# Optimization experiments

Hardware: AMD Instinct MI355X
Metric: run time of the kernel (lower is better)

The kernel has to match this reference:

```python
import jax, jax.numpy as jnp
import numpy as np

EMBED = 1024
HEADS = 16
HEAD_DIM = EMBED // HEADS
SCALING = HEAD_DIM ** -0.5
R = 16
LORA_SCALE = 32.0 / R  # alpha / r
NEG = jnp.finfo(jnp.float32).min


def lora_linear(x, W, A, B):
    # y = x @ W.T + (x @ A.T) @ B.T * scale   (LinearLora, bias=False)
    return x @ W.T + ((x @ A.T) @ B.T) * LORA_SCALE


def setup_inputs() -> dict:
    key = jax.random.key(0)
    ks = jax.random.split(key, 14)
    B, T, D = 1, 4096, EMBED
    hidden_states = jax.random.normal(ks[0], (B, T, D), jnp.float32)
    # causal additive mask (bsz, 1, tgt, src): 0 on/below diag, dtype-min above
    i = jnp.arange(T)
    causal = jnp.where(i[:, None] >= i[None, :], 0.0, NEG).astype(jnp.float32)
    attention_mask = jnp.broadcast_to(causal, (B, 1, T, T))
    s = 0.02
    def w(k, shape):
        return jax.random.normal(k, shape, jnp.float32) * s
    return dict(
        hidden_states=hidden_states,
        attention_mask=attention_mask,
        Wq=w(ks[1], (D, D)), Wk=w(ks[2], (D, D)), Wv=w(ks[3], (D, D)), Wo=w(ks[4], (D, D)),
        Aq=w(ks[5], (R, D)), Bq=jnp.zeros((D, R), jnp.float32) + w(ks[6], (D, R)),
        Ak=w(ks[7], (R, D)), Bk=w(ks[8], (D, R)),
        Av=w(ks[9], (R, D)), Bv=w(ks[10], (D, R)),
        Ao=w(ks[11], (R, D)), Bo=w(ks[12], (D, R)),
    )


def reference(hidden_states, attention_mask, Wq, Wk, Wv, Wo,
              Aq, Bq, Ak, Bk, Av, Bv, Ao, Bo):
    bsz, tgt_len, _ = hidden_states.shape
    H, Hd = HEADS, HEAD_DIM

    q = lora_linear(hidden_states, Wq, Aq, Bq) * SCALING
    k = lora_linear(hidden_states, Wk, Ak, Bk)
    v = lora_linear(hidden_states, Wv, Av, Bv)

    # (b, t, H, Hd)
    q = q.reshape(bsz, tgt_len, H, Hd)
    k = k.reshape(bsz, tgt_len, H, Hd)
    v = v.reshape(bsz, tgt_len, H, Hd)

    # scores (b, H, t, s)
    attn = jnp.einsum('bthd,bshd->bhts', q, k)
    attn = attn + attention_mask
    attn = jnp.maximum(attn, NEG)
    attn = jax.nn.softmax(attn, axis=-1)  # dropout p=0 / eval mode

    out = jnp.einsum('bhts,bshd->bthd', attn, v)
    out = out.reshape(bsz, tgt_len, H * Hd)
    out = lora_linear(out, Wo, Ao, Bo)
    return out
```

## Files before the change

kernel.cpp:

```cpp
#include <hip/hip_runtime.h>
#include <cmath>
#include <cstdint>

typedef unsigned short u16;
typedef __attribute__((ext_vector_type(8))) __bf16 bf16x8;
typedef __attribute__((ext_vector_type(4))) __bf16 bf16x4;
typedef __attribute__((ext_vector_type(4))) short s16x4;
typedef __attribute__((ext_vector_type(4))) float f32x4;

__device__ __forceinline__ u16 f2bf(float f) {
    union { float f; unsigned u; } v; v.f = f;
    unsigned r = v.u + 0x7fffu + ((v.u >> 16) & 1u);
    return (u16)(r >> 16);
}

__device__ __forceinline__ void gload_lds(const u16* g, u16* l) {
    __builtin_amdgcn_global_load_lds((__attribute__((address_space(1))) void*)g,
                                     (__attribute__((address_space(3))) void*)l,
                                     16, 0, 0);
}

__device__ __forceinline__ f32x4 mfma16(s16x4 a, s16x4 b, f32x4 c) {
#if __has_builtin(__builtin_amdgcn_mfma_f32_16x16x16bf16_1k)
    return __builtin_amdgcn_mfma_f32_16x16x16bf16_1k(a, b, c, 0, 0, 0);
#else
    asm("v_mfma_f32_16x16x16_bf16 %0, %1, %2, %3"
        : "=v"(c) : "v"(a), "v"(b), "0"(c));
    return c;
#endif
}

__global__ __launch_bounds__(256) void prep_all(
        const float* __restrict__ X,
        const float* __restrict__ Wq, const float* __restrict__ Wk,
        const float* __restrict__ Wv, const float* __restrict__ Wo,
        const float* __restrict__ Aq, const float* __restrict__ Bq,
        const float* __restrict__ Ak, const float* __restrict__ Bk,
        const float* __restrict__ Av, const float* __restrict__ Bv,
        const float* __restrict__ Ao, const float* __restrict__ Bo,
        u16* __restrict__ Wqkv, u16* __restrict__ Wob, u16* __restrict__ Xb) {
    const int p = blockIdx.y;
    const int idx = blockIdx.x * 256 + threadIdx.x;
    if (p == 4) {
        float4 v = ((const float4*)X)[idx];
        ushort4 o;
        o.x = f2bf(v.x); o.y = f2bf(v.y); o.z = f2bf(v.z); o.w = f2bf(v.w);
        ((ushort4*)Xb)[idx] = o;
        return;
    }
    const int n = idx >> 10, d = idx & 1023;
    const float* W; const float* A; const float* B;
    switch (p) {
        case 0: W = Wq; A = Aq; B = Bq; break;
        case 1: W = Wk; A = Ak; B = Bk; break;
        case 2: W = Wv; A = Av; B = Bv; break;
        default: W = Wo; A = Ao; B = Bo; break;
    }
    float lora = 0.f;
#pragma unroll
    for (int r = 0; r < 16; r++) lora += B[n * 16 + r] * A[r * 1024 + d];
    float v = W[idx] + 2.0f * lora;
    if (p == 0) v *= 0.125f * 1.44269504088896340736f;
    if (p < 3) Wqkv[(size_t)p * 1048576 + idx] = f2bf(v);
    else       Wob[idx] = f2bf(v);
}

template <bool F32OUT>
__global__ __launch_bounds__(256, 3) void gemm_bt(const u16* __restrict__ A,
                                                  const u16* __restrict__ B,
                                                  void* __restrict__ C, int ldc) {
    __shared__ __align__(16) u16 As[128 * 64];
    __shared__ __align__(16) u16 Bs[128 * 64];
    const int tid = threadIdx.x;
    const int lane = tid & 63, wave = tid >> 6;
    const int quad = lane >> 4, l16 = lane & 15;
    const int wm = (wave >> 1) * 64, wn = (wave & 1) * 64;
    const size_t m0 = (size_t)blockIdx.y * 128, n0 = (size_t)blockIdx.x * 128;
    const u16* Ap = A + m0 * 1024;
    const u16* Bp = B + n0 * 1024;
    const int xsw = l16 & 7;
    f32x4 acc[4][4] = {};
    for (int k0 = 0; k0 < 1024; k0 += 64) {
#pragma unroll
        for (int hh = 0; hh < 4; hh++) {
            int c = tid + hh * 256;
            int row = c >> 3, cg = (c & 7) ^ (row & 7);
            gload_lds(Ap + (size_t)row * 1024 + k0 + cg * 8, As + c * 8);
            gload_lds(Bp + (size_t)row * 1024 + k0 + cg * 8, Bs + c * 8);
        }
        asm volatile("s_waitcnt vmcnt(0)" ::: "memory");
        __syncthreads();
#pragma unroll
        for (int kf = 0; kf < 2; kf++) {
            bf16x8 af[4], bfr[4];
#pragma unroll
            for (int i = 0; i < 4; i++) {
                af[i]  = *(const bf16x8*)(As + (wm + i * 16 + l16) * 64
                                             + ((kf * 4 + quad) ^ xsw) * 8);
                bfr[i] = *(const bf16x8*)(Bs + (wn + i * 16 + l16) * 64
                                             + ((kf * 4 + quad) ^ xsw) * 8);
            }
#pragma unroll
            for (int mi = 0; mi < 4; mi++)
#pragma unroll
                for (int ni = 0; ni < 4; ni++)
                    acc[mi][ni] = __builtin_amdgcn_mfma_f32_16x16x32_bf16(
                            af[mi], bfr[ni], acc[mi][ni], 0, 0, 0);
        }
        __syncthreads();
    }
#pragma unroll
    for (int mi = 0; mi < 4; mi++)
#pragma unroll
        for (int ni = 0; ni < 4; ni++)
#pragma unroll
            for (int r = 0; r < 4; r++) {
                size_t row = m0 + wm + mi * 16 + quad * 4 + r;
                size_t col = n0 + wn + ni * 16 + l16;
                if (F32OUT) ((float*)C)[row * ldc + col] = acc[mi][ni][r];
                else        ((u16*)C)[row * ldc + col] = f2bf(acc[mi][ni][r]);
            }
}

template <bool F32OUT>
__global__ __launch_bounds__(256, 3) void gemm_bt64(const u16* __restrict__ A,
                                                    const u16* __restrict__ B,
                                                    void* __restrict__ C, int ldc) {
    __shared__ __align__(16) u16 As[64 * 64];
    __shared__ __align__(16) u16 Bs[128 * 64];
    const int tid = threadIdx.x;
    const int lane = tid & 63, wave = tid >> 6;
    const int quad = lane >> 4, l16 = lane & 15;
    const int wm = (wave >> 1) * 32, wn = (wave & 1) * 64;
    const size_t m0 = (size_t)blockIdx.y * 64, n0 = (size_t)blockIdx.x * 128;
    const u16* Ap = A + m0 * 1024;
    const u16* Bp = B + n0 * 1024;
    const int xsw = l16 & 7;
    f32x4 acc[2][4] = {};
    for (int k0 = 0; k0 < 1024; k0 += 64) {
#pragma unroll
        for (int hh = 0; hh < 2; hh++) {
            int c = tid + hh * 256;
            int row = c >> 3, cg = (c & 7) ^ (row & 7);
            gload_lds(Ap + (size_t)row * 1024 + k0 + cg * 8, As + c * 8);
        }
#pragma unroll
        for (int hh = 0; hh < 4; hh++) {
            int c = tid + hh * 256;
            int row = c >> 3, cg = (c & 7) ^ (row & 7);
            gload_lds(Bp + (size_t)row * 1024 + k0 + cg * 8, Bs + c * 8);
        }
        asm volatile("s_waitcnt vmcnt(0)" ::: "memory");
        __syncthreads();
#pragma unroll
        for (int kf = 0; kf < 2; kf++) {
            bf16x8 af[2], bfr[4];
#pragma unroll
            for (int i = 0; i < 2; i++)
                af[i] = *(const bf16x8*)(As + (wm + i * 16 + l16) * 64
                                            + ((kf * 4 + quad) ^ xsw) * 8);
#pragma unroll
            for (int i = 0; i < 4; i++)
                bfr[i] = *(const bf16x8*)(Bs + (wn + i * 16 + l16) * 64
                                             + ((kf * 4 + quad) ^ xsw) * 8);
#pragma unroll
            for (int mi = 0; mi < 2; mi++)
#pragma unroll
                for (int ni = 0; ni < 4; ni++)
                    acc[mi][ni] = __builtin_amdgcn_mfma_f32_16x16x32_bf16(
                            af[mi], bfr[ni], acc[mi][ni], 0, 0, 0);
        }
        __syncthreads();
    }
#pragma unroll
    for (int mi = 0; mi < 2; mi++)
#pragma unroll
        for (int ni = 0; ni < 4; ni++)
#pragma unroll
            for (int r = 0; r < 4; r++) {
                size_t row = m0 + wm + mi * 16 + quad * 4 + r;
                size_t col = n0 + wn + ni * 16 + l16;
                if (F32OUT) ((float*)C)[row * ldc + col] = acc[mi][ni][r];
                else        ((u16*)C)[row * ldc + col] = f2bf(acc[mi][ni][r]);
            }
}

__global__ __launch_bounds__(256) void transpose_v(const u16* __restrict__ Y,
                                                   u16* __restrict__ Vt) {
    __shared__ u16 tile[64][68];
    const int dv0 = blockIdx.x * 64;
    const int t0  = blockIdx.y * 64;
    const int tid = threadIdx.x;
#pragma unroll
    for (int p = 0; p < 4; p++) {
        int pos = tid + p * 256;
        int row = pos >> 4;
        int c4  = (pos & 15) * 4;
        ushort4 v = *(const ushort4*)(Y + (size_t)(t0 + row) * 3072 + 2048 + dv0 + c4);
        tile[row][c4 + 0] = v.x; tile[row][c4 + 1] = v.y;
        tile[row][c4 + 2] = v.z; tile[row][c4 + 3] = v.w;
    }
    __syncthreads();
#pragma unroll
    for (int p = 0; p < 4; p++) {
        int pos = tid + p * 256;
        int orow = pos >> 4;
        int oc4  = (pos & 15) * 4;
        ushort4 o;
        o.x = tile[oc4 + 0][orow]; o.y = tile[oc4 + 1][orow];
        o.z = tile[oc4 + 2][orow]; o.w = tile[oc4 + 3][orow];
        *(ushort4*)(Vt + (size_t)(dv0 + orow) * 4096 + t0 + oc4) = o;
    }
}

__global__ __launch_bounds__(256, 4) void flash_attn(const u16* __restrict__ Y,
                                                     const u16* __restrict__ Vt,
                                                     u16* __restrict__ O) {
    __shared__ __align__(16) u16 lds[16384];
    const int tid = threadIdx.x;
    const int wave = tid >> 6, lane = tid & 63;
    const int quad = lane >> 4, l16 = lane & 15;
    const int bid = blockIdx.x;
    const int rr = bid & 255, j = bid >> 8;
    const int b = rr >> 4, h = rr & 15;
    int p;
    switch (j) { case 0:  p = 63 - b; break;
                 case 1:  p = 32 + b; break;
                 case 2:  p = 31 - b; break;
                 default: p = b;      break; }
    const int q0 = p * 64;
    const int q0w = q0 + wave * 16;
    const int nT = p + 1;
    const u16* Kbase = Y + 1024 + h * 64;
    const u16* Vbase = Vt + (size_t)(h * 64) * 4096;
    const int xsw = l16 & 7;

    bf16x8 qf[2];
#pragma unroll
    for (int kf = 0; kf < 2; kf++)
        qf[kf] = *(const bf16x8*)(Y + (size_t)(q0w + l16) * 3072
                                    + h * 64 + kf * 32 + quad * 8);

    f32x4 oaccT[4] = {};
    f32x4 lacc = {};
    const s16x4 ones = { (short)0x3F80, (short)0x3F80,
                         (short)0x3F80, (short)0x3F80 };

#pragma unroll
    for (int pp = 0; pp < 2; pp++) {
        int c = pp * 256 + tid;
        int row = c >> 3, cg = (c & 7) ^ (row & 7);
        gload_lds(Kbase + (size_t)row * 3072 + cg * 8, lds + c * 8);
        gload_lds(Vbase + (size_t)row * 4096 + cg * 8, lds + 4096 + c * 8);
    }

#pragma unroll 1
    for (int t = 0; t < nT; t++) {
        const int s0 = t * 64;
        u16* Ks = lds + (t & 1) * 8192;
        u16* Vs = Ks + 4096;
        asm volatile("s_waitcnt vmcnt(0)" ::: "memory");
        __syncthreads();

        if (t + 1 < nT) {
            u16* Kn = lds + ((t + 1) & 1) * 8192;
            const int sn = s0 + 64;
#pragma unroll
            for (int pp = 0; pp < 2; pp++) {
                int c = pp * 256 + tid;
                int row = c >> 3, cg = (c & 7) ^ (row & 7);
                gload_lds(Kbase + (size_t)(sn + row) * 3072 + cg * 8, Kn + c * 8);
                gload_lds(Vbase + (size_t)row * 4096 + sn + cg * 8, Kn + 4096 + c * 8);
            }
        }

        bf16x8 kfr[4][2];
#pragma unroll
        for (int ni = 0; ni < 4; ni++) {
            int row = ni * 16 + l16;
            kfr[ni][0] = *(const bf16x8*)(Ks + row * 64 + ((quad) ^ xsw) * 8);
            kfr[ni][1] = *(const bf16x8*)(Ks + row * 64 + ((4 + quad) ^ xsw) * 8);
        }

        f32x4 sacc[4] = {};
#pragma unroll
        for (int ni = 0; ni < 4; ni++) {
            sacc[ni] = __builtin_amdgcn_mfma_f32_16x16x32_bf16(
                    kfr[ni][0], qf[0], sacc[ni], 0, 0, 0);
            sacc[ni] = __builtin_amdgcn_mfma_f32_16x16x32_bf16(
                    kfr[ni][1], qf[1], sacc[ni], 0, 0, 0);
        }

        s16x4 vfr[4][4];
#pragma unroll
        for (int nj = 0; nj < 4; nj++) {
            int row = nj * 16 + l16;
#pragma unroll
            for (int ni = 0; ni < 4; ni++) {
                int cc = ni * 2 + (quad >> 1);
                vfr[nj][ni] = *(const s16x4*)(Vs + row * 64 + (cc ^ xsw) * 8
                                                 + (quad & 1) * 4);
            }
        }

        const int qg = q0w + l16;
        const bool diag = (t == nT - 1);
#pragma unroll
        for (int ni = 0; ni < 4; ni++) {
            if (diag) {
#pragma unroll
                for (int r = 0; r < 4; r++) {
                    int sg = s0 + ni * 16 + quad * 4 + r;
                    if (sg > qg) sacc[ni][r] = -INFINITY;
                }
            }
            f32x4 pe;
#pragma unroll
            for (int r = 0; r < 4; r++)
                pe[r] = __builtin_amdgcn_exp2f(sacc[ni][r]);
            bf16x4 tt = { (__bf16)pe[0], (__bf16)pe[1],
                          (__bf16)pe[2], (__bf16)pe[3] };
            s16x4 pf = __builtin_bit_cast(s16x4, tt);
            lacc = mfma16(ones, pf, lacc);
#pragma unroll
            for (int nj = 0; nj < 4; nj++)
                oaccT[nj] = mfma16(vfr[nj][ni], pf, oaccT[nj]);
        }
    }

    __syncthreads();
    u16* scr = lds + wave * 1152;
    {
        float inv = 1.0f / lacc[0];
#pragma unroll
        for (int nj = 0; nj < 4; nj++) {
            bf16x4 t4 = { (__bf16)(oaccT[nj][0] * inv),
                          (__bf16)(oaccT[nj][1] * inv),
                          (__bf16)(oaccT[nj][2] * inv),
                          (__bf16)(oaccT[nj][3] * inv) };
            *(s16x4*)(scr + l16 * 72 + nj * 16 + quad * 4) =
                    __builtin_bit_cast(s16x4, t4);
        }
    }
    asm volatile("s_waitcnt lgkmcnt(0)" ::: "memory");
#pragma unroll
    for (int pp = 0; pp < 2; pp++) {
        int row = pp * 8 + (lane >> 3);
        int seg = (lane & 7) * 8;
        bf16x8 d = *(const bf16x8*)(scr + row * 72 + seg);
        *(bf16x8*)(O + (size_t)(q0w + row) * 1024 + h * 64 + seg) = d;
    }
}


extern "C" void kernel_launch(void* const* d_in, const int* in_sizes, int n_in,
                              void* d_out, int out_size, void* d_ws, size_t ws_size,
                              hipStream_t stream) {
    const float* X  = (const float*)d_in[0];
    const float* Wq = (const float*)d_in[2];
    const float* Wk = (const float*)d_in[3];
    const float* Wv = (const float*)d_in[4];
    const float* Wo = (const float*)d_in[5];
    const float* Aq = (const float*)d_in[6];
    const float* Bq = (const float*)d_in[7];
    const float* Ak = (const float*)d_in[8];
    const float* Bk = (const float*)d_in[9];
    const float* Av = (const float*)d_in[10];
    const float* Bv = (const float*)d_in[11];
    const float* Ao = (const float*)d_in[12];
    const float* Bo = (const float*)d_in[13];

    char* ws = (char*)d_ws;
    u16* Xb   = (u16*)(ws);
    u16* Wqkv = (u16*)(ws + (8u  << 20));
    u16* Wob  = (u16*)(ws + (14u << 20));
    u16* Y    = (u16*)(ws + (16u << 20));
    u16* Vt   = (u16*)(ws + (40u << 20));
    u16* Ob   = (u16*)(ws + (48u << 20));

    prep_all<<<dim3(4096, 5), 256, 0, stream>>>(X, Wq, Wk, Wv, Wo, Aq, Bq, Ak, Bk,
                                                Av, Bv, Ao, Bo, Wqkv, Wob, Xb);
    gemm_bt<false><<<dim3(24, 32), 256, 0, stream>>>(Xb, Wqkv, Y, 3072);
    transpose_v<<<dim3(16, 64), 256, 0, stream>>>(Y, Vt);
    flash_attn<<<dim3(1024), 256, 0, stream>>>(Y, Vt, Ob);
    gemm_bt64<true><<<dim3(8, 64), 256, 0, stream>>>(Ob, Wob, d_out, 1024);
}
```

Baseline: 256.6 us.

## Split long causal attention rows across two blocks with partial-sum combine kernel

Query tiles in the second half of the sequence are split over two blocks (key tiles 0-31 and 32-p), each writing unnormalized fp32 partial outputs and row sums to workspace. A new combine kernel adds the partials, normalizes and writes bf16. This shortens the longest blocks so work balances better across CUs, at the cost of extra fp32 traffic, an additional launch and workspace reuse of the Xb/Wqkv regions. No running max is tracked, so the partials can be summed directly.

Result: slower. 270.2 us (+5.3%).

```diff
diff --git a/kernel.cpp b/kernel.cpp
--- a/kernel.cpp
+++ b/kernel.cpp
@@ -213,24 +213,25 @@
     }
 }
 
-__global__ __launch_bounds__(256, 4) void flash_attn(const u16* __restrict__ Y,
-                                                     const u16* __restrict__ Vt,
-                                                     u16* __restrict__ O) {
+__global__ __launch_bounds__(256, 4) void flash_attn(
+        const u16* __restrict__ Y,
+        const u16* __restrict__ Vt,
+        u16* __restrict__ O,
+        float* __restrict__ OpA,
+        float* __restrict__ OpB,
+        float* __restrict__ lA,
+        float* __restrict__ lB) {
     __shared__ __align__(16) u16 lds[16384];
     const int tid = threadIdx.x;
     const int wave = tid >> 6, lane = tid & 63;
     const int quad = lane >> 4, l16 = lane & 15;
     const int bid = blockIdx.x;
-    const int rr = bid & 255, j = bid >> 8;
-    const int b = rr >> 4, h = rr & 15;
-    int p;
-    switch (j) { case 0:  p = 63 - b; break;
-                 case 1:  p = 32 + b; break;
-                 case 2:  p = 31 - b; break;
-                 default: p = b;      break; }
-    const int q0 = p * 64;
-    const int q0w = q0 + wave * 16;
-    const int nT = p + 1;
+    const int g = bid >> 4, h = bid & 15;
+    int p, t0, t1, mode;
+    if (g < 32)      { p = 32 + g;  t0 = 0;  t1 = 32;    mode = 1; }
+    else if (g < 64) { p = 63 - g;  t0 = 0;  t1 = p + 1; mode = 0; }
+    else             { p = 127 - g; t0 = 32; t1 = p + 1; mode = 2; }
+    const int q0w = p * 64 + wave * 16;
     const u16* Kbase = Y + 1024 + h * 64;
     const u16* Vbase = Vt + (size_t)(h * 64) * 4096;
     const int xsw = l16 & 7;
@@ -246,23 +247,27 @@
     const s16x4 ones = { (short)0x3F80, (short)0x3F80,
                          (short)0x3F80, (short)0x3F80 };
 
-#pragma unroll
-    for (int pp = 0; pp < 2; pp++) {
-        int c = pp * 256 + tid;
-        int row = c >> 3, cg = (c & 7) ^ (row & 7);
-        gload_lds(Kbase + (size_t)row * 3072 + cg * 8, lds + c * 8);
-        gload_lds(Vbase + (size_t)row * 4096 + cg * 8, lds + 4096 + c * 8);
+    {
+        const int s0p = t0 * 64;
+        u16* Kn = lds + (t0 & 1) * 8192;
+#pragma unroll
+        for (int pp = 0; pp < 2; pp++) {
+            int c = pp * 256 + tid;
+            int row = c >> 3, cg = (c & 7) ^ (row & 7);
+            gload_lds(Kbase + (size_t)(s0p + row) * 3072 + cg * 8, Kn + c * 8);
+            gload_lds(Vbase + (size_t)row * 4096 + s0p + cg * 8, Kn + 4096 + c * 8);
+        }
     }
 
 #pragma unroll 1
-    for (int t = 0; t < nT; t++) {
+    for (int t = t0; t < t1; t++) {
         const int s0 = t * 64;
         u16* Ks = lds + (t & 1) * 8192;
         u16* Vs = Ks + 4096;
         asm volatile("s_waitcnt vmcnt(0)" ::: "memory");
         __syncthreads();
 
-        if (t + 1 < nT) {
+        if (t + 1 < t1) {
             u16* Kn = lds + ((t + 1) & 1) * 8192;
             const int sn = s0 + 64;
 #pragma unroll
@@ -304,7 +309,7 @@
         }
 
         const int qg = q0w + l16;
-        const bool diag = (t == nT - 1);
+        const bool diag = (t == p);
 #pragma unroll
         for (int ni = 0; ni < 4; ni++) {
             if (diag) {
@@ -329,8 +334,8 @@
     }
 
     __syncthreads();
-    u16* scr = lds + wave * 1152;
-    {
+    if (mode == 0) {
+        u16* scr = lds + wave * 1152;
         float inv = 1.0f / lacc[0];
 #pragma unroll
         for (int nj = 0; nj < 4; nj++) {
@@ -341,15 +346,55 @@
             *(s16x4*)(scr + l16 * 72 + nj * 16 + quad * 4) =
                     __builtin_bit_cast(s16x4, t4);
         }
-    }
-    asm volatile("s_waitcnt lgkmcnt(0)" ::: "memory");
-#pragma unroll
-    for (int pp = 0; pp < 2; pp++) {
-        int row = pp * 8 + (lane >> 3);
-        int seg = (lane & 7) * 8;
-        bf16x8 d = *(const bf16x8*)(scr + row * 72 + seg);
-        *(bf16x8*)(O + (size_t)(q0w + row) * 1024 + h * 64 + seg) = d;
-    }
+        asm volatile("s_waitcnt lgkmcnt(0)" ::: "memory");
+#pragma unroll
+        for (int pp = 0; pp < 2; pp++) {
+            int row = pp * 8 + (lane >> 3);
+            int seg = (lane & 7) * 8;
+            bf16x8 d = *(const bf16x8*)(scr + row * 72 + seg);
+            *(bf16x8*)(O + (size_t)(q0w + row) * 1024 + h * 64 + seg) = d;
+        }
+    } else {
+        float* Op = (mode == 1) ? OpA : OpB;
+        float* lp = (mode == 1) ? lA : lB;
+        float* scr = (float*)lds + wave * 1088;
+#pragma unroll
+        for (int nj = 0; nj < 4; nj++)
+            *(f32x4*)(scr + l16 * 68 + nj * 16 + quad * 4) = oaccT[nj];
+        asm volatile("s_waitcnt lgkmcnt(0)" ::: "memory");
+#pragma unroll
+        for (int it = 0; it < 4; it++) {
+            int row = (lane >> 4) + it * 4;
+            int seg = (lane & 15) * 4;
+            f32x4 d = *(const f32x4*)(scr + row * 68 + seg);
+            *(f32x4*)(Op + (size_t)(q0w + row - 2048) * 1024 + h * 64 + seg) = d;
+        }
+        if (lane < 16)
+            lp[(size_t)(q0w + lane - 2048) * 16 + h] = lacc[0];
+    }
+}
+
+__global__ __launch_bounds__(256) void combine_o(
+        const float* __restrict__ OpA, const float* __restrict__ OpB,
+        const float* __restrict__ lA, const float* __restrict__ lB,
+        u16* __restrict__ O) {
+    const int idx = blockIdx.x * 256 + threadIdx.x;
+    const int r = idx >> 7;
+    const int c8 = (idx & 127) * 8;
+    const int h = c8 >> 6;
+    const float inv = 1.0f / (lA[r * 16 + h] + lB[r * 16 + h]);
+    const float* a = OpA + (size_t)r * 1024 + c8;
+    const float* b = OpB + (size_t)r * 1024 + c8;
+    float4 a0 = *(const float4*)a, a1 = *(const float4*)(a + 4);
+    float4 b0 = *(const float4*)b, b1 = *(const float4*)(b + 4);
+    ushort4 o0, o1;
+    o0.x = f2bf((a0.x + b0.x) * inv); o0.y = f2bf((a0.y + b0.y) * inv);
+    o0.z = f2bf((a0.z + b0.z) * inv); o0.w = f2bf((a0.w + b0.w) * inv);
+    o1.x = f2bf((a1.x + b1.x) * inv); o1.y = f2bf((a1.y + b1.y) * inv);
+    o1.z = f2bf((a1.z + b1.z) * inv); o1.w = f2bf((a1.w + b1.w) * inv);
+    u16* op = O + (size_t)(2048 + r) * 1024 + c8;
+    *(ushort4*)op = o0;
+    *(ushort4*)(op + 4) = o1;
 }
 
 
@@ -371,17 +416,22 @@
     const float* Bo = (const float*)d_in[13];
 
     char* ws = (char*)d_ws;
-    u16* Xb   = (u16*)(ws);
-    u16* Wqkv = (u16*)(ws + (8u  << 20));
-    u16* Wob  = (u16*)(ws + (14u << 20));
-    u16* Y    = (u16*)(ws + (16u << 20));
-    u16* Vt   = (u16*)(ws + (40u << 20));
-    u16* Ob   = (u16*)(ws + (48u << 20));
+    u16*   Xb   = (u16*)(ws);
+    float* OpA  = (float*)(ws);
+    u16*   Wqkv = (u16*)(ws + (8u  << 20));
+    float* OpB  = (float*)(ws + (8u  << 20));
+    float* lA   = (float*)(ws + (16u << 20));
+    float* lB   = (float*)(ws + (16u << 20) + (128u << 10));
+    u16*   Y    = (u16*)(ws + (17u << 20));
+    u16*   Vt   = (u16*)(ws + (41u << 20));
+    u16*   Ob   = (u16*)(ws + (49u << 20));
+    u16*   Wob  = (u16*)(ws + (57u << 20));
 
     prep_all<<<dim3(4096, 5), 256, 0, stream>>>(X, Wq, Wk, Wv, Wo, Aq, Bq, Ak, Bk,
                                                 Av, Bv, Ao, Bo, Wqkv, Wob, Xb);
     gemm_bt<false><<<dim3(24, 32), 256, 0, stream>>>(Xb, Wqkv, Y, 3072);
     transpose_v<<<dim3(16, 64), 256, 0, stream>>>(Y, Vt);
-    flash_attn<<<dim3(1024), 256, 0, stream>>>(Y, Vt, Ob);
+    flash_attn<<<dim3(1536), 256, 0, stream>>>(Y, Vt, Ob, OpA, OpB, lA, lB);
+    combine_o<<<dim3(1024), 256, 0, stream>>>(OpA, OpB, lA, lB, Ob);
     gemm_bt64<true><<<dim3(8, 64), 256, 0, stream>>>(Ob, Wob, d_out, 1024);
 }
```
